# Optimization experiments

Measured on AMD Instinct MI355X. Metric: run time of the kernel, lower is better.

## Reference

```python
import jax, jax.numpy as jnp
import numpy as np

B, N, D_MODEL, H, D_FF, NB_FEAT = 2, 2048, 512, 8, 2048, 256
DH = D_MODEL // H


def layer_norm(x, g, b, eps=1e-5):
    mu = jnp.mean(x, axis=-1, keepdims=True)
    var = jnp.mean((x - mu) ** 2, axis=-1, keepdims=True)
    return g * (x - mu) / jnp.sqrt(var + eps) + b


def softmax_kernel(data, proj, is_query, eps=1e-4):
    # Performer FAVOR+ positive random features. data: [b,h,n,dh], proj: [m,dh]
    dn = data.shape[-1] ** -0.25
    ratio = proj.shape[0] ** -0.5
    dd = jnp.einsum('bhnd,jd->bhnj', dn * data, proj)
    diag = (jnp.sum(data ** 2, axis=-1, keepdims=True) * 0.5) * (dn ** 2)
    if is_query:
        m = jnp.max(dd, axis=-1, keepdims=True)
    else:
        m = jnp.max(dd)
    return ratio * (jnp.exp(dd - diag - m) + eps)


def setup_inputs() -> dict:
    key = jax.random.key(0)
    ks = jax.random.split(key, 12)
    sd = D_MODEL ** -0.5
    sf = D_FF ** -0.5
    return {
        'x': jax.random.normal(ks[0], (B, N, D_MODEL), jnp.float32),
        'Wq': jax.random.normal(ks[1], (D_MODEL, D_MODEL), jnp.float32) * sd,
        'bq': jnp.zeros((D_MODEL,), jnp.float32),
        'Wk': jax.random.normal(ks[2], (D_MODEL, D_MODEL), jnp.float32) * sd,
        'bk': jnp.zeros((D_MODEL,), jnp.float32),
        'Wv': jax.random.normal(ks[3], (D_MODEL, D_MODEL), jnp.float32) * sd,
        'bv': jnp.zeros((D_MODEL,), jnp.float32),
        'Wo': jax.random.normal(ks[4], (D_MODEL, D_MODEL), jnp.float32) * sd,
        'bo': jnp.zeros((D_MODEL,), jnp.float32),
        'proj': jax.random.normal(ks[5], (NB_FEAT, DH), jnp.float32),
        'W1': jax.random.normal(ks[6], (D_MODEL, D_FF), jnp.float32) * sd,
        'b1': jnp.zeros((D_FF,), jnp.float32),
        'W2': jax.random.normal(ks[7], (D_FF, D_MODEL), jnp.float32) * sf,
        'b2': jnp.zeros((D_MODEL,), jnp.float32),
        'g1': jnp.ones((D_MODEL,), jnp.float32),
        'beta1': jnp.zeros((D_MODEL,), jnp.float32),
        'g2': jnp.ones((D_MODEL,), jnp.float32),
        'beta2': jnp.zeros((D_MODEL,), jnp.float32),
    }


def reference(x, Wq, bq, Wk, bk, Wv, bv, Wo, bo, proj, W1, b1, W2, b2, g1, beta1, g2, beta2):
    b, n, d = x.shape
    heads = lambda W, bias: (x @ W + bias).reshape(b, n, H, DH).transpose(0, 2, 1, 3)  # bhnd
    q = softmax_kernel(heads(Wq, bq), proj, is_query=True)   # [b,h,n,m]
    k = softmax_kernel(heads(Wk, bk), proj, is_query=False)  # [b,h,n,m]
    v = heads(Wv, bv)                                        # [b,h,n,dh]
    # non-causal linear attention
    k_sum = jnp.sum(k, axis=-2)                                   # [b,h,m]
    D_inv = 1.0 / jnp.einsum('bhnf,bhf->bhn', q, k_sum)           # [b,h,n]
    context = jnp.einsum('bhnf,bhne->bhfe', k, v)                 # [b,h,m,dh]
    out = jnp.einsum('bhfe,bhnf,bhn->bhne', context, q, D_inv)    # [b,h,n,dh]
    # output_attentions=True: effective attention matrix (abs, head-mean, detached)
    attn = jnp.einsum('bhnf,bhmf->bhnm', q, k) * D_inv[..., None]
    attn_weight = jax.lax.stop_gradient(jnp.mean(jnp.abs(attn), axis=1))  # [b,n,n]
    out = out.transpose(0, 2, 1, 3).reshape(b, n, d)
    out = out @ Wo + bo
    # NOTE: original module has no residual connections
    h1 = layer_norm(out, g1, beta1)
    ff = jax.nn.relu(h1 @ W1 + b1) @ W2 + b2
    y = layer_norm(ff, g2, beta2)
    return y, attn_weight
```

## Files before the change

kernel.cpp:

```cpp
#include <hip/hip_runtime.h>
#include <math.h>

#define B_SZ   2
#define N_TOK  2048
#define DM     512
#define NH     8
#define DHH    64
#define NF     256
#define DFF    2048
#define HF     2048
#define LDQKV  1536

constexpr float DN_SCALE   = 0.35355339059327373f;
constexpr float DIAG_SCALE = 0.0625f;
constexpr float RATIO      = 0.0625f;
constexpr float FEPS       = 1e-4f;
constexpr float LN_EPS     = 1e-5f;

typedef __attribute__((ext_vector_type(8))) short bf16x8;
typedef __attribute__((ext_vector_type(8))) _Float16 f16x8;
typedef __attribute__((ext_vector_type(4))) float f32x4;

__device__ __forceinline__ short f2b(float f) {
  union { float f; unsigned u; } x; x.f = f;
  unsigned r = (x.u + 0x7fff + ((x.u >> 16) & 1)) >> 16;
  return (short)r;
}
__device__ __forceinline__ float b2f(short s) {
  union { unsigned u; float f; } x; x.u = ((unsigned)(unsigned short)s) << 16;
  return x.f;
}
__device__ __forceinline__ void gload16(const void* g, void* l) {
  __builtin_amdgcn_global_load_lds((const __attribute__((address_space(1))) void*)g,
                                   (__attribute__((address_space(3))) void*)l, 16, 0, 0);
}
__device__ __forceinline__ int swz64(int row, int kbyte) {
  return (row * 128 + kbyte) ^ ((row & 7) << 4);
}

constexpr size_t OFF_S0    = 0;
constexpr size_t OFF_CTXP  = 0;
constexpr size_t OFF_QB    = 4194304;
constexpr size_t OFF_OUT2  = 0;
constexpr size_t OFF_FF1B  = 2097152;
constexpr size_t OFF_FF2   = 6291456;
constexpr size_t OFF_QFB   = 8388608;
constexpr size_t OFF_KB    = 12582912;
constexpr size_t OFF_QKV   = 16777216;
constexpr size_t OFF_AOB   = 20971520;
constexpr size_t OFF_H1B   = 22020096;
constexpr size_t OFF_WOT   = 23068672;
constexpr size_t OFF_W1T   = 23199744;
constexpr size_t OFF_W2T   = 23724032;
constexpr size_t OFF_KSUM  = 24248320;
constexpr size_t OFF_PART  = 24252416;
constexpr size_t OFF_DINV  = 24285184;
constexpr size_t OFF_CTXT  = 24317952;
constexpr size_t OFF_BMAX  = 24580096;
constexpr size_t OFF_GMAX  = 24612864;

template<bool RELU, bool OUT_BF16, bool HAS_BIAS, bool SWZ>
__global__ __launch_bounds__(256)
void gemm_mfma(const short* __restrict__ A, const short* __restrict__ Bt,
               const float* __restrict__ bias, void* __restrict__ Cout,
               int M, int N, int K, size_t sA, size_t sB, size_t sC, int ldC) {
  __shared__ short As[128 * 64];
  __shared__ short Bs[128 * 64];
  int tid = threadIdx.x;
  int lane = tid & 63, wave = tid >> 6;
  int wm = wave >> 1, wn = wave & 1;
  int bx = blockIdx.x, by = blockIdx.y;
  if (SWZ) {
    int nwg = gridDim.x * gridDim.y;
    int flat = by * gridDim.x + bx;
    int swz = (flat & 7) * (nwg >> 3) + (flat >> 3);
    bx = swz % gridDim.x; by = swz / gridDim.x;
  }
  int bm = by * 128, bn = bx * 128;
  const short* Ab = A + (size_t)blockIdx.z * sA;
  const short* Bb = Bt + (size_t)blockIdx.z * sB;

  f32x4 acc[4][4] = {};
  int srow = tid >> 3;
  int scol = (tid & 7) * 8;

  for (int k0 = 0; k0 < K; k0 += 64) {
    #pragma unroll
    for (int c = 0; c < 4; ++c) {
      int r = c * 32 + srow;
      gload16(Ab + (size_t)(bm + r) * K + k0 + scol, As + c * 2048 + wave * 512);
      gload16(Bb + (size_t)(bn + r) * K + k0 + scol, Bs + c * 2048 + wave * 512);
    }
    __syncthreads();
    #pragma unroll
    for (int kk = 0; kk < 2; ++kk) {
      bf16x8 af[4], bf[4];
      int kq = kk * 32 + (lane >> 4) * 8;
      #pragma unroll
      for (int i = 0; i < 4; ++i)
        af[i] = *(const bf16x8*)&As[(wm * 64 + i * 16 + (lane & 15)) * 64 + kq];
      #pragma unroll
      for (int j = 0; j < 4; ++j)
        bf[j] = *(const bf16x8*)&Bs[(wn * 64 + j * 16 + (lane & 15)) * 64 + kq];
      #pragma unroll
      for (int i = 0; i < 4; ++i)
        #pragma unroll
        for (int j = 0; j < 4; ++j)
          acc[i][j] = __builtin_amdgcn_mfma_f32_16x16x32_bf16(af[i], bf[j], acc[i][j], 0, 0, 0);
    }
    __syncthreads();
  }

  int row0 = bm + wm * 64, col0 = bn + wn * 64;
  #pragma unroll
  for (int i = 0; i < 4; ++i) {
    #pragma unroll
    for (int j = 0; j < 4; ++j) {
      int col = col0 + j * 16 + (lane & 15);
      float bv = HAS_BIAS ? bias[col] : 0.f;
      #pragma unroll
      for (int r = 0; r < 4; ++r) {
        int row = row0 + i * 16 + (lane >> 4) * 4 + r;
        float v = acc[i][j][r] + bv;
        if (RELU) v = fmaxf(v, 0.f);
        size_t off = (size_t)blockIdx.z * sC + (size_t)row * ldC + col;
        if (OUT_BF16) ((short*)Cout)[off] = f2b(v);
        else          ((float*)Cout)[off] = v;
      }
    }
  }
}

__global__ void cvt_bf16_kernel(const float* __restrict__ in, short* __restrict__ out) {
  size_t base = ((size_t)blockIdx.x * 256 + threadIdx.x) * 8;
  #pragma unroll
  for (int u = 0; u < 8; ++u) out[base + u] = f2b(in[base + u]);
}

__global__ void transpose_w4(const float* s0, const float* s1, const float* s2, const float* s3,
                             short* d0, short* d1, short* d2, short* d3) {
  __shared__ float t[64][65];
  int z = blockIdx.z;
  const float* W = (z == 0) ? s0 : (z == 1) ? s1 : (z == 2) ? s2 : s3;
  short* Wt      = (z == 0) ? d0 : (z == 1) ? d1 : (z == 2) ? d2 : d3;
  int k0 = blockIdx.y * 64, n0 = blockIdx.x * 64;
  int lx = threadIdx.x & 63, ly = threadIdx.x >> 6;
  for (int r = ly; r < 64; r += 4)
    t[r][lx] = W[(size_t)(k0 + r) * 512 + n0 + lx];
  __syncthreads();
  for (int r = ly; r < 64; r += 4)
    Wt[(size_t)(n0 + r) * 512 + k0 + lx] = f2b(t[lx][r]);
}

__global__ void transpose_w(const float* __restrict__ W, short* __restrict__ Wt, int K, int N) {
  __shared__ float t[64][65];
  int k0 = blockIdx.y * 64, n0 = blockIdx.x * 64;
  int lx = threadIdx.x & 63, ly = threadIdx.x >> 6;
  for (int r = ly; r < 64; r += 4)
    t[r][lx] = W[(size_t)(k0 + r) * N + n0 + lx];
  __syncthreads();
  for (int r = ly; r < 64; r += 4)
    Wt[(size_t)(n0 + r) * K + k0 + lx] = f2b(t[lx][r]);
}

template<bool IS_QUERY>
__global__ __launch_bounds__(256)
void feat_mfma_kernel(const float* __restrict__ qkv, int coff, const float* __restrict__ bias,
                      const float* __restrict__ proj, short* __restrict__ qfb,
                      float* __restrict__ ktmp, float* __restrict__ bmax) {
  __shared__ short qh[64 * 64], ql[64 * 64];
  __shared__ short ph[128 * 64], pl[128 * 64];
  __shared__ float dpart[64][4];
  __shared__ float diag[64];
  __shared__ float wred[4];
  int t = threadIdx.x;
  int bh = blockIdx.y, b = bh >> 3, h = bh & 7;
  int n0 = blockIdx.x * 64;
  int lane = t & 63, w = t >> 6, l15 = lane & 15, lq = lane >> 4;

  {
    int r = t >> 2, cg = (t & 3) * 16;
    const float* src = qkv + (size_t)(b * N_TOK + n0 + r) * LDQKV + coff + h * 64 + cg;
    const float* bs = bias + h * 64 + cg;
    float ss = 0.f;
    #pragma unroll
    for (int c2 = 0; c2 < 2; ++c2) {
      f16x8 H, L;
      #pragma unroll
      for (int u = 0; u < 8; ++u) {
        float xv = src[c2 * 8 + u] + bs[c2 * 8 + u];
        ss += xv * xv;
        _Float16 hi = (_Float16)xv;
        H[u] = hi;
        L[u] = (_Float16)(xv - (float)hi);
      }
      int off = swz64(r, cg * 2 + c2 * 16);
      *(f16x8*)((char*)qh + off) = H;
      *(f16x8*)((char*)ql + off) = L;
    }
    dpart[r][t & 3] = ss;
  }
  __syncthreads();
  if (t < 64)
    diag[t] = (dpart[t][0] + dpart[t][1] + dpart[t][2] + dpart[t][3]) * DIAG_SCALE;

  f16x8 ah[2], al[2];
  #pragma unroll
  for (int kk = 0; kk < 2; ++kk) {
    int off = swz64(w * 16 + l15, kk * 64 + lq * 16);
    ah[kk] = *(f16x8*)((char*)qh + off);
    al[kk] = *(f16x8*)((char*)ql + off);
  }

  f32x4 acc[16] = {};
  #pragma unroll
  for (int half = 0; half < 2; ++half) {
    __syncthreads();
    {
      int r = t & 127, cg = (t >> 7) * 32;
      const float* src = proj + (size_t)(half * 128 + r) * DHH + cg;
      #pragma unroll
      for (int c2 = 0; c2 < 4; ++c2) {
        f16x8 H, L;
        #pragma unroll
        for (int u = 0; u < 8; ++u) {
          float xv = src[c2 * 8 + u];
          _Float16 hi = (_Float16)xv;
          H[u] = hi;
          L[u] = (_Float16)(xv - (float)hi);
        }
        int off = swz64(r, cg * 2 + c2 * 16);
        *(f16x8*)((char*)ph + off) = H;
        *(f16x8*)((char*)pl + off) = L;
      }
    }
    __syncthreads();
    #pragma unroll
    for (int jl = 0; jl < 8; ++jl) {
      int row = jl * 16 + l15;
      #pragma unroll
      for (int kk = 0; kk < 2; ++kk) {
        int off = swz64(row, kk * 64 + lq * 16);
        f16x8 bh8 = *(f16x8*)((char*)ph + off);
        f16x8 bl8 = *(f16x8*)((char*)pl + off);
        acc[half * 8 + jl] = __builtin_amdgcn_mfma_f32_16x16x32_f16(ah[kk], bh8, acc[half * 8 + jl], 0, 0, 0);
        acc[half * 8 + jl] = __builtin_amdgcn_mfma_f32_16x16x32_f16(al[kk], bh8, acc[half * 8 + jl], 0, 0, 0);
        acc[half * 8 + jl] = __builtin_amdgcn_mfma_f32_16x16x32_f16(ah[kk], bl8, acc[half * 8 + jl], 0, 0, 0);
      }
    }
  }

  if (IS_QUERY) {
    #pragma unroll
    for (int r = 0; r < 4; ++r) {
      float mx = -3.4e38f;
      #pragma unroll
      for (int j = 0; j < 16; ++j) mx = fmaxf(mx, acc[j][r]);
      #pragma unroll
      for (int o = 1; o < 16; o <<= 1) mx = fmaxf(mx, __shfl_xor(mx, o, 64));
      int lrow = w * 16 + lq * 4 + r;
      float dg = diag[lrow];
      float ddm = mx * DN_SCALE;
      size_t base = (size_t)(b * N_TOK + n0 + lrow) * HF + h * NF + l15;
      #pragma unroll
      for (int j = 0; j < 16; ++j) {
        float v = RATIO * (expf(acc[j][r] * DN_SCALE - dg - ddm) + FEPS);
        qfb[base + j * 16] = f2b(v);
      }
    }
  } else {
    float mxall = -3.4e38f;
    #pragma unroll
    for (int r = 0; r < 4; ++r) {
      int lrow = w * 16 + lq * 4 + r;
      float dg = diag[lrow];
      size_t base = (size_t)(b * N_TOK + n0 + lrow) * HF + h * NF + l15;
      #pragma unroll
      for (int j = 0; j < 16; ++j) {
        float a = acc[j][r];
        mxall = fmaxf(mxall, a);
        ktmp[base + j * 16] = expf(a * DN_SCALE - dg);
      }
    }
    #pragma unroll
    for (int o = 1; o < 64; o <<= 1) mxall = fmaxf(mxall, __shfl_xor(mxall, o, 64));
    if (lane == 0) wred[w] = mxall;
    __syncthreads();
    if (t == 0)
      bmax[bh * 32 + blockIdx.x] =
          fmaxf(fmaxf(wred[0], wred[1]), fmaxf(wred[2], wred[3])) * DN_SCALE;
  }
}

__global__ void gmax_kernel(const float* __restrict__ bmax, float* __restrict__ gmax) {
  __shared__ float red[4];
  float m = -3.4e38f;
  for (int i = threadIdx.x; i < 512; i += 256) m = fmaxf(m, bmax[i]);
  #pragma unroll
  for (int o = 32; o > 0; o >>= 1) m = fmaxf(m, __shfl_xor(m, o, 64));
  if ((threadIdx.x & 63) == 0) red[threadIdx.x >> 6] = m;
  __syncthreads();
  if (threadIdx.x == 0) gmax[0] = fmaxf(fmaxf(red[0], red[1]), fmaxf(red[2], red[3]));
}

__global__ void featk2_kernel(const float* __restrict__ ktmp, const float* __restrict__ gmax,
                              short* __restrict__ kb) {
  size_t base = ((size_t)blockIdx.x * 256 + threadIdx.x) * 8;
  float s = expf(-gmax[0]);
  #pragma unroll
  for (int u = 0; u < 8; ++u)
    kb[base + u] = f2b(RATIO * (ktmp[base + u] * s + FEPS));
}

__global__ void ksum_part_kernel(const short* __restrict__ kb, float* __restrict__ part) {
  int f = threadIdx.x, chunk = blockIdx.x, bh = blockIdx.y;
  int b = bh >> 3, h = bh & 7;
  int n0 = chunk * 256;
  float s = 0.f;
  for (int n = n0; n < n0 + 256; ++n)
    s += b2f(kb[(size_t)(b * N_TOK + n) * HF + h * NF + f]);
  part[(size_t)(bh * 8 + chunk) * NF + f] = s;
}

__global__ void ksum_final_kernel(const float* __restrict__ part, float* __restrict__ ksum) {
  int f = threadIdx.x, bh = blockIdx.x;
  float s = 0.f;
  #pragma unroll
  for (int c = 0; c < 8; ++c) s += part[(size_t)(bh * 8 + c) * NF + f];
  ksum[bh * NF + f] = s;
}

__global__ __launch_bounds__(256)
void dinvqs_kernel(const short* __restrict__ qfb, const float* __restrict__ ksum,
                   float* __restrict__ Dinv, short* __restrict__ qb) {
  int R = blockIdx.x;
  int b = R >> 11, n = R & 2047;
  int t = threadIdx.x;
  bf16x8 qv = *(const bf16x8*)(qfb + (size_t)R * HF + t * 8);
  const float* ks = ksum + b * 2048 + t * 8;
  float p = 0.f;
  #pragma unroll
  for (int u = 0; u < 8; ++u) p += b2f(qv[u]) * ks[u];
  #pragma unroll
  for (int o = 1; o < 32; o <<= 1) p += __shfl_xor(p, o, 64);
  float d = 1.0f / p;
  if ((t & 31) == 0) Dinv[(b * NH + (t >> 5)) * N_TOK + n] = d;
  float dv = d * 0.125f;
  bf16x8 o8;
  #pragma unroll
  for (int u = 0; u < 8; ++u) o8[u] = f2b(b2f(qv[u]) * dv);
  *(bf16x8*)(qb + (size_t)R * HF + t * 8) = o8;
}

__global__ __launch_bounds__(256)
void ctx_part_kernel(const short* __restrict__ kb, const float* __restrict__ qkv,
                     const float* __restrict__ bv, float* __restrict__ ctxp) {
  int bh = blockIdx.y, b = bh >> 3, h = bh & 7;
  int f0 = blockIdx.x * 64;
  int ns = blockIdx.z * 128;
  __shared__ float kf[32][68];
  __shared__ float vs[32][68];
  int tid = threadIdx.x;
  int tf = (tid >> 4) * 4, te = (tid & 15) * 4;
  float acc[4][4] = {};
  for (int n0 = ns; n0 < ns + 128; n0 += 32) {
    #pragma unroll
    for (int i = 0; i < 8; i++) {
      int idx = tid + i * 256;
      int nn = idx >> 6, f = idx & 63;
      kf[nn][f] = b2f(kb[(size_t)(b * N_TOK + n0 + nn) * HF + h * NF + f0 + f]);
    }
    #pragma unroll
    for (int i = 0; i < 8; i++) {
      int idx = tid + i * 256;
      int nn = idx >> 6, e = idx & 63;
      vs[nn][e] = qkv[(size_t)(b * N_TOK + n0 + nn) * LDQKV + 1024 + h * DHH + e] + bv[h * DHH + e];
    }
    __syncthreads();
    #pragma unroll
    for (int nn = 0; nn < 32; nn++) {
      float a[4], bb[4];
      #pragma unroll
      for (int i = 0; i < 4; i++) a[i] = kf[nn][tf + i];
      #pragma unroll
      for (int j = 0; j < 4; j++) bb[j] = vs[nn][te + j];
      #pragma unroll
      for (int i = 0; i < 4; i++)
        #pragma unroll
        for (int j = 0; j < 4; j++) acc[i][j] += a[i] * bb[j];
    }
    __syncthreads();
  }
  #pragma unroll
  for (int i = 0; i < 4; i++)
    #pragma unroll
    for (int j = 0; j < 4; j++)
      ctxp[(size_t)blockIdx.z * 262144 + (size_t)bh * 16384 +
           (size_t)(f0 + tf + i) * 64 + te + j] = acc[i][j];
}

__global__ __launch_bounds__(256)
void ctx_reduce_kernel(const float* __restrict__ ctxp, short* __restrict__ ctxT) {
  __shared__ float T[64][65];
  int ftile = blockIdx.x, bh = blockIdx.y;
  int tid = threadIdx.x;
  int e = tid & 63, q = tid >> 6;
  #pragma unroll
  for (int i = 0; i < 16; ++i) {
    int fl = i * 4 + q;
    size_t idx = (size_t)bh * 16384 + (size_t)(ftile * 64 + fl) * 64 + e;
    float s = 0.f;
    #pragma unroll
    for (int c = 0; c < 16; ++c) s += ctxp[(size_t)c * 262144 + idx];
    T[fl][e] = s;
  }
  __syncthreads();
  #pragma unroll
  for (int i = 0; i < 16; ++i) {
    int er = i * 4 + q;
    ctxT[(size_t)bh * 16384 + (size_t)er * 256 + ftile * 64 + e] = f2b(T[e][er]);
  }
}

__global__ __launch_bounds__(256)
void pv_mfma_kernel(const short* __restrict__ qfb, const short* __restrict__ ctxT,
                    const float* __restrict__ Dinv, short* __restrict__ aob) {
  __shared__ short As[128 * 64];
  __shared__ short Bs[64 * 64];
  int bh = blockIdx.y, b = bh >> 3, h = bh & 7;
  int n0 = blockIdx.x * 128;
  int tid = threadIdx.x;
  int lane = tid & 63, wave = tid >> 6;
  int srow = tid >> 3, scol = (tid & 7) * 8;

  f32x4 acc[2][4] = {};
  for (int k0 = 0; k0 < NF; k0 += 64) {
    #pragma unroll
    for (int c = 0; c < 4; ++c) {
      int r = c * 32 + srow;
      gload16(qfb + (size_t)(b * N_TOK + n0 + r) * HF + h * NF + k0 + scol,
              As + c * 2048 + wave * 512);
    }
    #pragma unroll
    for (int c = 0; c < 2; ++c) {
      int r = c * 32 + srow;
      gload16(ctxT + (size_t)bh * 16384 + (size_t)r * 256 + k0 + scol,
              Bs + c * 2048 + wave * 512);
    }
    __syncthreads();
    #pragma unroll
    for (int kk = 0; kk < 2; ++kk) {
      bf16x8 af[2], bf[4];
      int kq = kk * 32 + (lane >> 4) * 8;
      #pragma unroll
      for (int i = 0; i < 2; ++i)
        af[i] = *(const bf16x8*)&As[(wave * 32 + i * 16 + (lane & 15)) * 64 + kq];
      #pragma unroll
      for (int j = 0; j < 4; ++j)
        bf[j] = *(const bf16x8*)&Bs[(j * 16 + (lane & 15)) * 64 + kq];
      #pragma unroll
      for (int i = 0; i < 2; ++i)
        #pragma unroll
        for (int j = 0; j < 4; ++j)
          acc[i][j] = __builtin_amdgcn_mfma_f32_16x16x32_bf16(af[i], bf[j], acc[i][j], 0, 0, 0);
    }
    __syncthreads();
  }

  #pragma unroll
  for (int i = 0; i < 2; ++i) {
    #pragma unroll
    for (int j = 0; j < 4; ++j) {
      int e = j * 16 + (lane & 15);
      #pragma unroll
      for (int r = 0; r < 4; ++r) {
        int n = n0 + wave * 32 + i * 16 + (lane >> 4) * 4 + r;
        float dv = Dinv[bh * N_TOK + n];
        aob[(size_t)(b * N_TOK + n) * DM + h * DHH + e] = f2b(acc[i][j][r] * dv);
      }
    }
  }
}

template<bool OUT_BF16>
__global__ void ln_kernel(const float* __restrict__ x, const float* __restrict__ g,
                          const float* __restrict__ beta, void* __restrict__ y) {
  int row = blockIdx.x, t = threadIdx.x;
  __shared__ float red[4];
  __shared__ float bcast[2];
  const float* xr = x + (size_t)row * DM;
  float v0 = xr[t], v1 = xr[t + 256];
  float s = v0 + v1;
  #pragma unroll
  for (int o = 32; o > 0; o >>= 1) s += __shfl_xor(s, o, 64);
  if ((t & 63) == 0) red[t >> 6] = s;
  __syncthreads();
  if (t == 0) bcast[0] = (red[0] + red[1] + red[2] + red[3]) * (1.0f / 512.0f);
  __syncthreads();
  float mean = bcast[0];
  float d0 = v0 - mean, d1 = v1 - mean;
  float s2 = d0 * d0 + d1 * d1;
  #pragma unroll
  for (int o = 32; o > 0; o >>= 1) s2 += __shfl_xor(s2, o, 64);
  if ((t & 63) == 0) red[t >> 6] = s2;
  __syncthreads();
  if (t == 0) bcast[1] = (red[0] + red[1] + red[2] + red[3]) * (1.0f / 512.0f);
  __syncthreads();
  float inv = rsqrtf(bcast[1] + LN_EPS);
  float o0 = g[t] * d0 * inv + beta[t];
  float o1 = g[t + 256] * d1 * inv + beta[t + 256];
  if (OUT_BF16) {
    ((short*)y)[(size_t)row * DM + t] = f2b(o0);
    ((short*)y)[(size_t)row * DM + t + 256] = f2b(o1);
  } else {
    ((float*)y)[(size_t)row * DM + t] = o0;
    ((float*)y)[(size_t)row * DM + t + 256] = o1;
  }
}

extern "C" void kernel_launch(void* const* d_in, const int* in_sizes, int n_in,
                              void* d_out, int out_size, void* d_ws, size_t ws_size,
                              hipStream_t stream) {
  const float* x     = (const float*)d_in[0];
  const float* Wq    = (const float*)d_in[1];
  const float* bq    = (const float*)d_in[2];
  const float* Wk    = (const float*)d_in[3];
  const float* bk    = (const float*)d_in[4];
  const float* Wv    = (const float*)d_in[5];
  const float* bv    = (const float*)d_in[6];
  const float* Wo    = (const float*)d_in[7];
  const float* bo    = (const float*)d_in[8];
  const float* proj  = (const float*)d_in[9];
  const float* W1    = (const float*)d_in[10];
  const float* b1    = (const float*)d_in[11];
  const float* W2    = (const float*)d_in[12];
  const float* b2    = (const float*)d_in[13];
  const float* g1    = (const float*)d_in[14];
  const float* beta1 = (const float*)d_in[15];
  const float* g2    = (const float*)d_in[16];
  const float* beta2 = (const float*)d_in[17];

  float* ws = (float*)d_ws;
  float* y_out = (float*)d_out;
  float* attnw = y_out + (size_t)B_SZ * N_TOK * DM;

  float* ktmp  = ws + OFF_S0;
  float* ctxp  = ws + OFF_CTXP;
  short* qb    = (short*)(ws + OFF_QB);
  float* out2  = ws + OFF_OUT2;
  short* ff1b  = (short*)(ws + OFF_FF1B);
  float* ff2   = ws + OFF_FF2;
  short* qfb   = (short*)(ws + OFF_QFB);
  short* xb    = (short*)(ws + OFF_QFB);
  short* kb    = (short*)(ws + OFF_KB);
  short* Wqkvt = (short*)(ws + OFF_KB);
  float* QKVlin = ws + OFF_QKV;
  short* aob   = (short*)(ws + OFF_AOB);
  short* h1b   = (short*)(ws + OFF_H1B);
  short* Wot   = (short*)(ws + OFF_WOT);
  short* W1t   = (short*)(ws + OFF_W1T);
  short* W2t   = (short*)(ws + OFF_W2T);
  float* ksum  = ws + OFF_KSUM;
  float* part  = ws + OFF_PART;
  float* Dinv  = ws + OFF_DINV;
  short* ctxT  = (short*)(ws + OFF_CTXT);
  float* bmax  = ws + OFF_BMAX;
  float* gmax  = ws + OFF_GMAX;

  dim3 blk(256);
  int MT = B_SZ * N_TOK;

  cvt_bf16_kernel<<<(MT * DM) / (256 * 8), blk, 0, stream>>>(x, xb);
  transpose_w4<<<dim3(8, 8, 4), blk, 0, stream>>>(
      Wq, Wk, Wv, Wo, Wqkvt, Wqkvt + 262144, Wqkvt + 524288, Wot);
  transpose_w<<<dim3(32, 8), blk, 0, stream>>>(W1, W1t, DM, DFF);
  transpose_w<<<dim3(8, 32), blk, 0, stream>>>(W2, W2t, DFF, DM);

  gemm_mfma<false, false, false, false><<<dim3(LDQKV / 128, MT / 128, 1), blk, 0, stream>>>(
      xb, Wqkvt, nullptr, QKVlin, MT, LDQKV, DM, 0, 0, 0, LDQKV);

  feat_mfma_kernel<true><<<dim3(N_TOK / 64, B_SZ * NH), blk, 0, stream>>>(
      QKVlin, 0, bq, proj, qfb, nullptr, nullptr);
  feat_mfma_kernel<false><<<dim3(N_TOK / 64, B_SZ * NH), blk, 0, stream>>>(
      QKVlin, 512, bk, proj, nullptr, ktmp, bmax);
  gmax_kernel<<<1, blk, 0, stream>>>(bmax, gmax);
  featk2_kernel<<<(B_SZ * N_TOK * HF) / (256 * 8), blk, 0, stream>>>(ktmp, gmax, kb);

  ksum_part_kernel<<<dim3(8, B_SZ * NH), blk, 0, stream>>>(kb, part);
  ksum_final_kernel<<<B_SZ * NH, blk, 0, stream>>>(part, ksum);
  dinvqs_kernel<<<MT, blk, 0, stream>>>(qfb, ksum, Dinv, qb);

  ctx_part_kernel<<<dim3(NF / 64, B_SZ * NH, 16), blk, 0, stream>>>(kb, QKVlin, bv, ctxp);
  ctx_reduce_kernel<<<dim3(4, B_SZ * NH), blk, 0, stream>>>(ctxp, ctxT);
  pv_mfma_kernel<<<dim3(N_TOK / 128, B_SZ * NH), blk, 0, stream>>>(qfb, ctxT, Dinv, aob);

  gemm_mfma<false, false, false, true><<<dim3(16, 16, 2), blk, 0, stream>>>(
      qb, kb, nullptr, attnw, N_TOK, N_TOK, HF,
      (size_t)N_TOK * HF, (size_t)N_TOK * HF, (size_t)N_TOK * N_TOK, N_TOK);

  gemm_mfma<false, false, true, false><<<dim3(4, 32, 1), blk, 0, stream>>>(
      aob, Wot, bo, out2, MT, DM, DM, 0, 0, 0, DM);

  ln_kernel<true><<<MT, blk, 0, stream>>>(out2, g1, beta1, h1b);
  gemm_mfma<true, true, true, false><<<dim3(16, 32, 1), blk, 0, stream>>>(
      h1b, W1t, b1, ff1b, MT, DFF, DM, 0, 0, 0, DFF);
  gemm_mfma<false, false, true, false><<<dim3(4, 32, 1), blk, 0, stream>>>(
      ff1b, W2t, b2, ff2, MT, DM, DFF, 0, 0, 0, DM);
  ln_kernel<false><<<MT, blk, 0, stream>>>(ff2, g2, beta2, y_out);
}
```

Baseline: 271.3 us.

## Fold global key max into downstream scales and fuse prep, ksum and feature passes

```diff
diff --git a/kernel.cpp b/kernel.cpp
--- a/kernel.cpp
+++ b/kernel.cpp
@@ -53,13 +53,15 @@
 constexpr size_t OFF_W1T   = 23199744;
 constexpr size_t OFF_W2T   = 23724032;
 constexpr size_t OFF_KSUM  = 24248320;
-constexpr size_t OFF_PART  = 24252416;
-constexpr size_t OFF_DINV  = 24285184;
-constexpr size_t OFF_CTXT  = 24317952;
-constexpr size_t OFF_BMAX  = 24580096;
-constexpr size_t OFF_GMAX  = 24612864;
-
-template<bool RELU, bool OUT_BF16, bool HAS_BIAS, bool SWZ>
+constexpr size_t OFF_DINV  = 24252416;
+constexpr size_t OFF_CTXT  = 24285184;
+constexpr size_t OFF_BMAX  = 24416256;
+constexpr size_t OFF_GMAX  = 24416768;
+constexpr size_t OFF_ROWC  = 24416832;
+constexpr size_t OFF_PART  = 24420928;
+constexpr size_t OFF_VSUMP = 24552000;
+
+template<bool RELU, bool OUT_BF16, int BMODE, bool SWZ>
 __global__ __launch_bounds__(256)
 void gemm_mfma(const short* __restrict__ A, const short* __restrict__ Bt,
                const float* __restrict__ bias, void* __restrict__ Cout,
@@ -79,6 +81,7 @@
   int bm = by * 128, bn = bx * 128;
   const short* Ab = A + (size_t)blockIdx.z * sA;
   const short* Bb = Bt + (size_t)blockIdx.z * sB;
+  const float* rc = (BMODE == 2) ? (bias + (size_t)blockIdx.z * M) : bias;
 
   f32x4 acc[4][4] = {};
   int srow = tid >> 3;
@@ -117,11 +120,12 @@
     #pragma unroll
     for (int j = 0; j < 4; ++j) {
       int col = col0 + j * 16 + (lane & 15);
-      float bv = HAS_BIAS ? bias[col] : 0.f;
+      float bv = (BMODE == 1) ? rc[col] : 0.f;
       #pragma unroll
       for (int r = 0; r < 4; ++r) {
         int row = row0 + i * 16 + (lane >> 4) * 4 + r;
         float v = acc[i][j][r] + bv;
+        if (BMODE == 2) v += rc[row];
         if (RELU) v = fmaxf(v, 0.f);
         size_t off = (size_t)blockIdx.z * sC + (size_t)row * ldC + col;
         if (OUT_BF16) ((short*)Cout)[off] = f2b(v);
@@ -131,31 +135,88 @@
   }
 }
 
-__global__ void cvt_bf16_kernel(const float* __restrict__ in, short* __restrict__ out) {
-  size_t base = ((size_t)blockIdx.x * 256 + threadIdx.x) * 8;
-  #pragma unroll
-  for (int u = 0; u < 8; ++u) out[base + u] = f2b(in[base + u]);
-}
-
-__global__ void transpose_w4(const float* s0, const float* s1, const float* s2, const float* s3,
-                             short* d0, short* d1, short* d2, short* d3) {
+template<bool RELU, bool OUT_BF16>
+__global__ __launch_bounds__(256)
+void gemm_bn64(const short* __restrict__ A, const short* __restrict__ Bt,
+               const float* __restrict__ bias, void* __restrict__ Cout,
+               int M, int N, int K) {
+  __shared__ short As[128 * 64];
+  __shared__ short Bs[64 * 64];
+  int tid = threadIdx.x, lane = tid & 63, wave = tid >> 6;
+  int bn = blockIdx.x * 64, bm = blockIdx.y * 128;
+  int srow = tid >> 3, scol = (tid & 7) * 8;
+  f32x4 acc[2][4] = {};
+  for (int k0 = 0; k0 < K; k0 += 64) {
+    #pragma unroll
+    for (int c = 0; c < 4; ++c)
+      gload16(A + (size_t)(bm + c * 32 + srow) * K + k0 + scol, As + c * 2048 + wave * 512);
+    #pragma unroll
+    for (int c = 0; c < 2; ++c)
+      gload16(Bt + (size_t)(bn + c * 32 + srow) * K + k0 + scol, Bs + c * 2048 + wave * 512);
+    __syncthreads();
+    #pragma unroll
+    for (int kk = 0; kk < 2; ++kk) {
+      bf16x8 af[2], bf[4];
+      int kq = kk * 32 + (lane >> 4) * 8;
+      #pragma unroll
+      for (int i = 0; i < 2; ++i)
+        af[i] = *(const bf16x8*)&As[(wave * 32 + i * 16 + (lane & 15)) * 64 + kq];
+      #pragma unroll
+      for (int j = 0; j < 4; ++j)
+        bf[j] = *(const bf16x8*)&Bs[(j * 16 + (lane & 15)) * 64 + kq];
+      #pragma unroll
+      for (int i = 0; i < 2; ++i)
+        #pragma unroll
+        for (int j = 0; j < 4; ++j)
+          acc[i][j] = __builtin_amdgcn_mfma_f32_16x16x32_bf16(af[i], bf[j], acc[i][j], 0, 0, 0);
+    }
+    __syncthreads();
+  }
+  #pragma unroll
+  for (int i = 0; i < 2; ++i) {
+    #pragma unroll
+    for (int j = 0; j < 4; ++j) {
+      int col = bn + j * 16 + (lane & 15);
+      float bv = bias[col];
+      #pragma unroll
+      for (int r = 0; r < 4; ++r) {
+        int row = bm + wave * 32 + i * 16 + (lane >> 4) * 4 + r;
+        float v = acc[i][j][r] + bv;
+        if (RELU) v = fmaxf(v, 0.f);
+        if (OUT_BF16) ((short*)Cout)[(size_t)row * N + col] = f2b(v);
+        else          ((float*)Cout)[(size_t)row * N + col] = v;
+      }
+    }
+  }
+}
+
+__global__ void prep_kernel(const float* __restrict__ x, short* __restrict__ xb,
+                            const float* Wq, const float* Wk, const float* Wv, const float* Wo,
+                            short* Wqt, short* Wkt, short* Wvt, short* Wot,
+                            const float* W1, short* W1t, const float* W2, short* W2t) {
   __shared__ float t[64][65];
-  int z = blockIdx.z;
-  const float* W = (z == 0) ? s0 : (z == 1) ? s1 : (z == 2) ? s2 : s3;
-  short* Wt      = (z == 0) ? d0 : (z == 1) ? d1 : (z == 2) ? d2 : d3;
-  int k0 = blockIdx.y * 64, n0 = blockIdx.x * 64;
-  int lx = threadIdx.x & 63, ly = threadIdx.x >> 6;
-  for (int r = ly; r < 64; r += 4)
-    t[r][lx] = W[(size_t)(k0 + r) * 512 + n0 + lx];
-  __syncthreads();
-  for (int r = ly; r < 64; r += 4)
-    Wt[(size_t)(n0 + r) * 512 + k0 + lx] = f2b(t[lx][r]);
-}
-
-__global__ void transpose_w(const float* __restrict__ W, short* __restrict__ Wt, int K, int N) {
-  __shared__ float t[64][65];
-  int k0 = blockIdx.y * 64, n0 = blockIdx.x * 64;
-  int lx = threadIdx.x & 63, ly = threadIdx.x >> 6;
+  int id = blockIdx.x, tid = threadIdx.x;
+  if (id >= 768) {
+    size_t base = ((size_t)(id - 768) * 256 + tid) * 8;
+    #pragma unroll
+    for (int u = 0; u < 8; ++u) xb[base + u] = f2b(x[base + u]);
+    return;
+  }
+  const float* W; short* Wt; int K, N, bx, by;
+  if (id < 256) {
+    int z = id >> 6, sub = id & 63;
+    W  = (z == 0) ? Wq : (z == 1) ? Wk : (z == 2) ? Wv : Wo;
+    Wt = (z == 0) ? Wqt : (z == 1) ? Wkt : (z == 2) ? Wvt : Wot;
+    K = 512; N = 512; bx = sub & 7; by = sub >> 3;
+  } else if (id < 512) {
+    int sub = id - 256;
+    W = W1; Wt = W1t; K = 512; N = 2048; bx = sub & 31; by = sub >> 5;
+  } else {
+    int sub = id - 512;
+    W = W2; Wt = W2t; K = 2048; N = 512; bx = sub & 7; by = sub >> 3;
+  }
+  int k0 = by * 64, n0 = bx * 64;
+  int lx = tid & 63, ly = tid >> 6;
   for (int r = ly; r < 64; r += 4)
     t[r][lx] = W[(size_t)(k0 + r) * N + n0 + lx];
   __syncthreads();
@@ -166,13 +227,14 @@
 template<bool IS_QUERY>
 __global__ __launch_bounds__(256)
 void feat_mfma_kernel(const float* __restrict__ qkv, int coff, const float* __restrict__ bias,
-                      const float* __restrict__ proj, short* __restrict__ qfb,
-                      float* __restrict__ ktmp, float* __restrict__ bmax) {
+                      const float* __restrict__ proj, short* __restrict__ qout,
+                      float* __restrict__ part, float* __restrict__ bmax) {
   __shared__ short qh[64 * 64], ql[64 * 64];
   __shared__ short ph[128 * 64], pl[128 * 64];
   __shared__ float dpart[64][4];
   __shared__ float diag[64];
   __shared__ float wred[4];
+  __shared__ float colp[4][256];
   int t = threadIdx.x;
   int bh = blockIdx.y, b = bh >> 3, h = bh & 7;
   int n0 = blockIdx.x * 64;
@@ -265,11 +327,14 @@
       #pragma unroll
       for (int j = 0; j < 16; ++j) {
         float v = RATIO * (expf(acc[j][r] * DN_SCALE - dg - ddm) + FEPS);
-        qfb[base + j * 16] = f2b(v);
+        qout[base + j * 16] = f2b(v);
       }
     }
   } else {
     float mxall = -3.4e38f;
+    float cs[16];
+    #pragma unroll
+    for (int j = 0; j < 16; ++j) cs[j] = 0.f;
     #pragma unroll
     for (int r = 0; r < 4; ++r) {
       int lrow = w * 16 + lq * 4 + r;
@@ -279,63 +344,63 @@
       for (int j = 0; j < 16; ++j) {
         float a = acc[j][r];
         mxall = fmaxf(mxall, a);
-        ktmp[base + j * 16] = expf(a * DN_SCALE - dg);
-      }
+        float e = expf(a * DN_SCALE - dg);
+        cs[j] += e;
+        qout[base + j * 16] = f2b(e);
+      }
+    }
+    #pragma unroll
+    for (int j = 0; j < 16; ++j) {
+      cs[j] += __shfl_xor(cs[j], 16, 64);
+      cs[j] += __shfl_xor(cs[j], 32, 64);
+    }
+    if (lq == 0) {
+      #pragma unroll
+      for (int j = 0; j < 16; ++j) colp[w][j * 16 + l15] = cs[j];
     }
     #pragma unroll
     for (int o = 1; o < 64; o <<= 1) mxall = fmaxf(mxall, __shfl_xor(mxall, o, 64));
     if (lane == 0) wred[w] = mxall;
     __syncthreads();
+    part[(size_t)(bh * 32 + blockIdx.x) * 256 + t] =
+        colp[0][t] + colp[1][t] + colp[2][t] + colp[3][t];
     if (t == 0)
       bmax[bh * 32 + blockIdx.x] =
           fmaxf(fmaxf(wred[0], wred[1]), fmaxf(wred[2], wred[3])) * DN_SCALE;
   }
 }
 
-__global__ void gmax_kernel(const float* __restrict__ bmax, float* __restrict__ gmax) {
+__global__ void ksum_final_kernel(const float* __restrict__ part, const float* __restrict__ bmax,
+                                  float* __restrict__ ksum, float* __restrict__ gmax) {
   __shared__ float red[4];
-  float m = -3.4e38f;
-  for (int i = threadIdx.x; i < 512; i += 256) m = fmaxf(m, bmax[i]);
-  #pragma unroll
-  for (int o = 32; o > 0; o >>= 1) m = fmaxf(m, __shfl_xor(m, o, 64));
-  if ((threadIdx.x & 63) == 0) red[threadIdx.x >> 6] = m;
-  __syncthreads();
-  if (threadIdx.x == 0) gmax[0] = fmaxf(fmaxf(red[0], red[1]), fmaxf(red[2], red[3]));
-}
-
-__global__ void featk2_kernel(const float* __restrict__ ktmp, const float* __restrict__ gmax,
-                              short* __restrict__ kb) {
-  size_t base = ((size_t)blockIdx.x * 256 + threadIdx.x) * 8;
-  float s = expf(-gmax[0]);
-  #pragma unroll
-  for (int u = 0; u < 8; ++u)
-    kb[base + u] = f2b(RATIO * (ktmp[base + u] * s + FEPS));
-}
-
-__global__ void ksum_part_kernel(const short* __restrict__ kb, float* __restrict__ part) {
-  int f = threadIdx.x, chunk = blockIdx.x, bh = blockIdx.y;
-  int b = bh >> 3, h = bh & 7;
-  int n0 = chunk * 256;
-  float s = 0.f;
-  for (int n = n0; n < n0 + 256; ++n)
-    s += b2f(kb[(size_t)(b * N_TOK + n) * HF + h * NF + f]);
-  part[(size_t)(bh * 8 + chunk) * NF + f] = s;
-}
-
-__global__ void ksum_final_kernel(const float* __restrict__ part, float* __restrict__ ksum) {
-  int f = threadIdx.x, bh = blockIdx.x;
-  float s = 0.f;
-  #pragma unroll
-  for (int c = 0; c < 8; ++c) s += part[(size_t)(bh * 8 + c) * NF + f];
-  ksum[bh * NF + f] = s;
+  __shared__ float bc[1];
+  int bh = blockIdx.x, t = threadIdx.x;
+  float m = fmaxf(bmax[t], bmax[t + 256]);
+  #pragma unroll
+  for (int o = 1; o < 64; o <<= 1) m = fmaxf(m, __shfl_xor(m, o, 64));
+  if ((t & 63) == 0) red[t >> 6] = m;
+  __syncthreads();
+  if (t == 0) {
+    bc[0] = fmaxf(fmaxf(red[0], red[1]), fmaxf(red[2], red[3]));
+    if (bh == 0) gmax[0] = bc[0];
+  }
+  __syncthreads();
+  float s = expf(-bc[0]);
+  float sum = 0.f;
+  #pragma unroll 8
+  for (int c = 0; c < 32; ++c) sum += part[(size_t)(bh * 32 + c) * 256 + t];
+  ksum[bh * 256 + t] = RATIO * (s * sum + (float)N_TOK * FEPS);
 }
 
 __global__ __launch_bounds__(256)
 void dinvqs_kernel(const short* __restrict__ qfb, const float* __restrict__ ksum,
-                   float* __restrict__ Dinv, short* __restrict__ qb) {
+                   const float* __restrict__ gmax, float* __restrict__ Dinv,
+                   float* __restrict__ rowc, short* __restrict__ qb) {
+  __shared__ float wsum[4];
   int R = blockIdx.x;
   int b = R >> 11, n = R & 2047;
   int t = threadIdx.x;
+  float sc = RATIO * expf(-gmax[0]);
   bf16x8 qv = *(const bf16x8*)(qfb + (size_t)R * HF + t * 8);
   const float* ks = ksum + b * 2048 + t * 8;
   float p = 0.f;
@@ -346,24 +411,36 @@
   float d = 1.0f / p;
   if ((t & 31) == 0) Dinv[(b * NH + (t >> 5)) * N_TOK + n] = d;
   float dv = d * 0.125f;
+  float qs = 0.f;
   bf16x8 o8;
   #pragma unroll
-  for (int u = 0; u < 8; ++u) o8[u] = f2b(b2f(qv[u]) * dv);
+  for (int u = 0; u < 8; ++u) {
+    float qb_f = b2f(qv[u]) * dv;
+    qs += qb_f;
+    o8[u] = f2b(qb_f * sc);
+  }
   *(bf16x8*)(qb + (size_t)R * HF + t * 8) = o8;
+  #pragma unroll
+  for (int o = 1; o < 64; o <<= 1) qs += __shfl_xor(qs, o, 64);
+  if ((t & 63) == 0) wsum[t >> 6] = qs;
+  __syncthreads();
+  if (t == 0) rowc[R] = RATIO * FEPS * (wsum[0] + wsum[1] + wsum[2] + wsum[3]);
 }
 
 __global__ __launch_bounds__(256)
 void ctx_part_kernel(const short* __restrict__ kb, const float* __restrict__ qkv,
-                     const float* __restrict__ bv, float* __restrict__ ctxp) {
+                     const float* __restrict__ bv, float* __restrict__ ctxp,
+                     float* __restrict__ vsump) {
   int bh = blockIdx.y, b = bh >> 3, h = bh & 7;
   int f0 = blockIdx.x * 64;
-  int ns = blockIdx.z * 128;
+  int ns = blockIdx.z * 256;
   __shared__ float kf[32][68];
   __shared__ float vs[32][68];
   int tid = threadIdx.x;
   int tf = (tid >> 4) * 4, te = (tid & 15) * 4;
   float acc[4][4] = {};
-  for (int n0 = ns; n0 < ns + 128; n0 += 32) {
+  float vloc[4] = {};
+  for (int n0 = ns; n0 < ns + 256; n0 += 32) {
     #pragma unroll
     for (int i = 0; i < 8; i++) {
       int idx = tid + i * 256;
@@ -389,6 +466,14 @@
         #pragma unroll
         for (int j = 0; j < 4; j++) acc[i][j] += a[i] * bb[j];
     }
+    if (blockIdx.x == 0 && (tid >> 4) == 0) {
+      #pragma unroll
+      for (int j = 0; j < 4; j++) {
+        float s = 0.f;
+        for (int nn = 0; nn < 32; nn++) s += vs[nn][te + j];
+        vloc[j] += s;
+      }
+    }
     __syncthreads();
   }
   #pragma unroll
@@ -397,22 +482,32 @@
     for (int j = 0; j < 4; j++)
       ctxp[(size_t)blockIdx.z * 262144 + (size_t)bh * 16384 +
            (size_t)(f0 + tf + i) * 64 + te + j] = acc[i][j];
+  if (blockIdx.x == 0 && (tid >> 4) == 0) {
+    #pragma unroll
+    for (int j = 0; j < 4; j++)
+      vsump[((size_t)blockIdx.z * 16 + bh) * 64 + te + j] = vloc[j];
+  }
 }
 
 __global__ __launch_bounds__(256)
-void ctx_reduce_kernel(const float* __restrict__ ctxp, short* __restrict__ ctxT) {
+void ctx_reduce_kernel(const float* __restrict__ ctxp, const float* __restrict__ vsump,
+                       const float* __restrict__ gmax, short* __restrict__ ctxT) {
   __shared__ float T[64][65];
   int ftile = blockIdx.x, bh = blockIdx.y;
   int tid = threadIdx.x;
   int e = tid & 63, q = tid >> 6;
+  float s = expf(-gmax[0]);
+  float vsum_e = 0.f;
+  #pragma unroll
+  for (int c = 0; c < 8; ++c) vsum_e += vsump[((size_t)c * 16 + bh) * 64 + e];
   #pragma unroll
   for (int i = 0; i < 16; ++i) {
     int fl = i * 4 + q;
     size_t idx = (size_t)bh * 16384 + (size_t)(ftile * 64 + fl) * 64 + e;
-    float s = 0.f;
-    #pragma unroll
-    for (int c = 0; c < 16; ++c) s += ctxp[(size_t)c * 262144 + idx];
-    T[fl][e] = s;
+    float sum = 0.f;
+    #pragma unroll
+    for (int c = 0; c < 8; ++c) sum += ctxp[(size_t)c * 262144 + idx];
+    T[fl][e] = RATIO * (s * sum + FEPS * vsum_e);
   }
   __syncthreads();
   #pragma unroll
@@ -544,7 +639,6 @@
   float* y_out = (float*)d_out;
   float* attnw = y_out + (size_t)B_SZ * N_TOK * DM;
 
-  float* ktmp  = ws + OFF_S0;
   float* ctxp  = ws + OFF_CTXP;
   short* qb    = (short*)(ws + OFF_QB);
   float* out2  = ws + OFF_OUT2;
@@ -561,50 +655,47 @@
   short* W1t   = (short*)(ws + OFF_W1T);
   short* W2t   = (short*)(ws + OFF_W2T);
   float* ksum  = ws + OFF_KSUM;
-  float* part  = ws + OFF_PART;
   float* Dinv  = ws + OFF_DINV;
   short* ctxT  = (short*)(ws + OFF_CTXT);
   float* bmax  = ws + OFF_BMAX;
   float* gmax  = ws + OFF_GMAX;
+  float* rowc  = ws + OFF_ROWC;
+  float* part  = ws + OFF_PART;
+  float* vsump = ws + OFF_VSUMP;
 
   dim3 blk(256);
   int MT = B_SZ * N_TOK;
 
-  cvt_bf16_kernel<<<(MT * DM) / (256 * 8), blk, 0, stream>>>(x, xb);
-  transpose_w4<<<dim3(8, 8, 4), blk, 0, stream>>>(
-      Wq, Wk, Wv, Wo, Wqkvt, Wqkvt + 262144, Wqkvt + 524288, Wot);
-  transpose_w<<<dim3(32, 8), blk, 0, stream>>>(W1, W1t, DM, DFF);
-  transpose_w<<<dim3(8, 32), blk, 0, stream>>>(W2, W2t, DFF, DM);
-
-  gemm_mfma<false, false, false, false><<<dim3(LDQKV / 128, MT / 128, 1), blk, 0, stream>>>(
+  prep_kernel<<<1792, blk, 0, stream>>>(x, xb, Wq, Wk, Wv, Wo,
+                                        Wqkvt, Wqkvt + 262144, Wqkvt + 524288, Wot,
+                                        W1, W1t, W2, W2t);
+
+  gemm_mfma<false, false, 0, false><<<dim3(LDQKV / 128, MT / 128, 1), blk, 0, stream>>>(
       xb, Wqkvt, nullptr, QKVlin, MT, LDQKV, DM, 0, 0, 0, LDQKV);
 
   feat_mfma_kernel<true><<<dim3(N_TOK / 64, B_SZ * NH), blk, 0, stream>>>(
       QKVlin, 0, bq, proj, qfb, nullptr, nullptr);
   feat_mfma_kernel<false><<<dim3(N_TOK / 64, B_SZ * NH), blk, 0, stream>>>(
-      QKVlin, 512, bk, proj, nullptr, ktmp, bmax);
-  gmax_kernel<<<1, blk, 0, stream>>>(bmax, gmax);
-  featk2_kernel<<<(B_SZ * N_TOK * HF) / (256 * 8), blk, 0, stream>>>(ktmp, gmax, kb);
-
-  ksum_part_kernel<<<dim3(8, B_SZ * NH), blk, 0, stream>>>(kb, part);
-  ksum_final_kernel<<<B_SZ * NH, blk, 0, stream>>>(part, ksum);
-  dinvqs_kernel<<<MT, blk, 0, stream>>>(qfb, ksum, Dinv, qb);
-
-  ctx_part_kernel<<<dim3(NF / 64, B_SZ * NH, 16), blk, 0, stream>>>(kb, QKVlin, bv, ctxp);
-  ctx_reduce_kernel<<<dim3(4, B_SZ * NH), blk, 0, stream>>>(ctxp, ctxT);
+      QKVlin, 512, bk, proj, kb, part, bmax);
+
+  ksum_final_kernel<<<B_SZ * NH, blk, 0, stream>>>(part, bmax, ksum, gmax);
+  dinvqs_kernel<<<MT, blk, 0, stream>>>(qfb, ksum, gmax, Dinv, rowc, qb);
+
+  ctx_part_kernel<<<dim3(NF / 64, B_SZ * NH, 8), blk, 0, stream>>>(kb, QKVlin, bv, ctxp, vsump);
+  ctx_reduce_kernel<<<dim3(4, B_SZ * NH), blk, 0, stream>>>(ctxp, vsump, gmax, ctxT);
   pv_mfma_kernel<<<dim3(N_TOK / 128, B_SZ * NH), blk, 0, stream>>>(qfb, ctxT, Dinv, aob);
 
-  gemm_mfma<false, false, false, true><<<dim3(16, 16, 2), blk, 0, stream>>>(
-      qb, kb, nullptr, attnw, N_TOK, N_TOK, HF,
+  gemm_mfma<false, false, 2, true><<<dim3(16, 16, 2), blk, 0, stream>>>(
+      qb, kb, rowc, attnw, N_TOK, N_TOK, HF,
       (size_t)N_TOK * HF, (size_t)N_TOK * HF, (size_t)N_TOK * N_TOK, N_TOK);
 
-  gemm_mfma<false, false, true, false><<<dim3(4, 32, 1), blk, 0, stream>>>(
-      aob, Wot, bo, out2, MT, DM, DM, 0, 0, 0, DM);
+  gemm_bn64<false, false><<<dim3(DM / 64, MT / 128), blk, 0, stream>>>(
+      aob, Wot, bo, out2, MT, DM, DM);
 
   ln_kernel<true><<<MT, blk, 0, stream>>>(out2, g1, beta1, h1b);
-  gemm_mfma<true, true, true, false><<<dim3(16, 32, 1), blk, 0, stream>>>(
+  gemm_mfma<true, true, 1, false><<<dim3(16, 32, 1), blk, 0, stream>>>(
       h1b, W1t, b1, ff1b, MT, DFF, DM, 0, 0, 0, DFF);
-  gemm_mfma<false, false, true, false><<<dim3(4, 32, 1), blk, 0, stream>>>(
-      ff1b, W2t, b2, ff2, MT, DM, DFF, 0, 0, 0, DM);
+  gemm_bn64<false, false><<<dim3(DM / 64, MT / 128), blk, 0, stream>>>(
+      ff1b, W2t, b2, ff2, MT, DM, DFF);
   ln_kernel<false><<<MT, blk, 0, stream>>>(ff2, g2, beta2, y_out);
 }
```

Result: faster. 263.6 us (-2.8%).
